# Kernel tuning notes

Hardware: AMD Instinct MI355X
Metric: run time of the kernel (lower is better)

The kernel has to match this reference:

```python
import jax, jax.numpy as jnp
import numpy as np

N_STATES = 12
N_SUBJECTS = 100
N_CHANNELS = 64
BATCH = 32
SEQ = 1024
LAMBDA_MU = 1.0
LAMBDA_L = 1.0


def _make_chol(key, shape):
    # valid lower-triangular Cholesky factors with positive diagonal
    a = jax.random.normal(key, shape, dtype=jnp.float32) * 0.05
    eye = jnp.eye(shape[-1], dtype=jnp.float32)
    return jnp.tril(a) + eye


def setup_inputs() -> dict:
    key = jax.random.key(0)
    ks = jax.random.split(key, 7)
    data = jax.random.normal(ks[0], (BATCH, SEQ, N_CHANNELS), dtype=jnp.float32)
    mu_pop = jax.random.normal(ks[1], (N_STATES, N_CHANNELS), dtype=jnp.float32)
    L_pop = _make_chol(ks[2], (N_STATES, N_CHANNELS, N_CHANNELS))
    mu_subj = jax.random.normal(ks[3], (N_SUBJECTS, N_STATES, N_CHANNELS), dtype=jnp.float32)
    L_subj = _make_chol(ks[4], (N_SUBJECTS, N_STATES, N_CHANNELS, N_CHANNELS))
    gamma = jax.random.uniform(ks[5], (BATCH, SEQ, N_STATES), dtype=jnp.float32)
    gamma = gamma / jnp.sum(gamma, axis=-1, keepdims=True)  # responsibilities sum to 1
    subject_ids = jax.random.randint(ks[6], (BATCH, 1), 0, N_SUBJECTS, dtype=jnp.int32)
    return {"data": data, "mu_pop": mu_pop, "L_pop": L_pop,
            "mu_subj": mu_subj, "L_subj": L_subj, "gamma": gamma,
            "subject_ids": subject_ids}


def reference(data, mu_pop, L_pop, mu_subj, L_subj, gamma, subject_ids):
    sid = subject_ids.reshape(-1).astype(jnp.int32)            # (B,)
    mu_b = mu_subj[sid]                                        # (B,K,C)
    L_b = L_subj[sid]                                          # (B,K,C,C)

    C = data.shape[-1]
    # diff[b,k,c,t] = data[b,t,c] - mu_b[b,k,c]  -> (B,K,C,T)
    diff = jnp.transpose(data, (0, 2, 1))[:, None, :, :] - mu_b[:, :, :, None]
    # batched triangular solve: z = L^{-1} diff  (B,K,C,T)
    z = jax.lax.linalg.triangular_solve(L_b, diff, left_side=True, lower=True)
    quad = jnp.sum(z * z, axis=2)                              # (B,K,T)
    logdet = jnp.sum(jnp.log(jnp.diagonal(L_b, axis1=-2, axis2=-1)), axis=-1)  # (B,K)
    log_2pi = jnp.float32(np.log(2.0 * np.pi))
    log_probs = -0.5 * quad - logdet[:, :, None] - 0.5 * C * log_2pi  # (B,K,T)

    weighted_ll = jnp.einsum('btk,bkt->bt', gamma, log_probs)  # (B,T)
    # calculation == 'sum': sum over time, mean over batch
    ll = jnp.mean(jnp.sum(weighted_ll, axis=1))
    nll = -ll

    n_total = jnp.float32(mu_subj.shape[0])
    present = jnp.zeros((mu_subj.shape[0],), dtype=jnp.float32).at[sid].set(1.0)
    mu_reg = jnp.sum(present * jnp.sum((mu_subj - mu_pop[None]) ** 2, axis=(1, 2)))
    L_reg = jnp.sum(present * jnp.sum((L_subj - L_pop[None]) ** 2, axis=(1, 2, 3)))
    scale = jnp.sum(present) / n_total
    reg = (LAMBDA_MU / 2.0 * mu_reg + LAMBDA_L / 2.0 * L_reg) * scale

    total = nll + reg
    return total[None]  # shape (1,), matching tf.expand_dims(total_loss, -1)
```

## Files before the change

### kernel.cpp

```cpp
#include <hip/hip_runtime.h>
#include <math.h>

#define NB 32
#define NT 1024
#define NK 12
#define NC 64
#define NS 100
#define SOLVE_BLOCKS (NB * NK * 4)
#define REG_BLOCKS (NS * NK)


__global__ __launch_bounds__(128) void init_kernel(int* __restrict__ present) {
  int tid = threadIdx.x;
  if (tid < NS) present[tid] = 0;
}

template <int C>
struct Row {
  static __device__ __forceinline__ void run(float (&z)[NC],
                                             const float4* __restrict__ Ls4,
                                             float& quad) {
    float a0 = z[C];
    float a1 = 0.0f;
    float diag = 0.0f;
#pragma unroll
    for (int g = 0; g <= C / 4; ++g) {
      float4 v = Ls4[C * 16 + g];
#pragma unroll
      for (int e = 0; e < 4; ++e) {
        int j = 4 * g + e;
        float ve = (e == 0) ? v.x : (e == 1) ? v.y : (e == 2) ? v.z : v.w;
        if (j < C) {
          if (j & 1)
            a1 = fmaf(-ve, z[j], a1);
          else
            a0 = fmaf(-ve, z[j], a0);
        } else if (j == C) {
          diag = ve;
        }
      }
    }
    float zc = (a0 + a1) * __builtin_amdgcn_rcpf(diag);
    z[C] = zc;
    quad = fmaf(zc, zc, quad);
    Row<C + 1>::run(z, Ls4, quad);
  }
};
template <>
struct Row<NC> {
  static __device__ __forceinline__ void run(float (&)[NC], const float4*,
                                             float&) {}
};

__global__ __launch_bounds__(256) void solve_kernel(
    const float* __restrict__ data,
    const float* __restrict__ mu_subj,
    const float* __restrict__ L_subj,
    const float* __restrict__ gamma,
    const int*   __restrict__ sids,
    float*       __restrict__ solve_part,
    int*         __restrict__ present) {
  int blk  = blockIdx.x;
  int x    = blk & 7;
  int r    = blk >> 3;
  int b    = (r / 48) * 8 + x;
  int kt   = r % 48;
  int k    = kt >> 2;
  int tile = kt & 3;
  int tid  = threadIdx.x;
  int lane = tid & 63;
  int t    = tile * 256 + tid;

  int sid = __builtin_amdgcn_readfirstlane(sids[b]);
  if (tid == 0 && k == 0 && tile == 0) present[sid] = 1;

  const float* __restrict__ Lb = L_subj + (size_t)(sid * NK + k) * (NC * NC);
  const float* __restrict__ mu = mu_subj + (size_t)(sid * NK + k) * NC;

  __shared__ float4 Ls4[NC * NC / 4];
  const float4* Lg = reinterpret_cast<const float4*>(Lb);
#pragma unroll
  for (int i = 0; i < 4; ++i) Ls4[tid + 256 * i] = Lg[tid + 256 * i];
  __syncthreads();

  const float* Lsf = reinterpret_cast<const float*>(Ls4);
  float ld = __logf(Lsf[lane * (NC + 1)]);
#pragma unroll
  for (int off = 1; off < 64; off <<= 1) ld += __shfl_xor(ld, off);

  float z[NC];
  const float4* dp =
      reinterpret_cast<const float4*>(data + ((size_t)b * NT + t) * NC);
#pragma unroll
  for (int i = 0; i < NC / 4; ++i) {
    float4 v = dp[i];
    z[4 * i + 0] = v.x - mu[4 * i + 0];
    z[4 * i + 1] = v.y - mu[4 * i + 1];
    z[4 * i + 2] = v.z - mu[4 * i + 2];
    z[4 * i + 3] = v.w - mu[4 * i + 3];
  }

  float quad = 0.0f;
  Row<0>::run(z, Ls4, quad);

  float g = gamma[((size_t)b * NT + t) * NK + k];
  float w = g * (-0.5f * quad - ld);

#pragma unroll
  for (int off = 1; off < 64; off <<= 1) w += __shfl_xor(w, off);

  __shared__ float red[4];
  if (lane == 0) red[tid >> 6] = w;
  __syncthreads();
  if (tid == 0) solve_part[blockIdx.x] = red[0] + red[1] + red[2] + red[3];
}

__global__ __launch_bounds__(256) void reg_kernel(
    const float* __restrict__ mu_pop,
    const float* __restrict__ L_pop,
    const float* __restrict__ mu_subj,
    const float* __restrict__ L_subj,
    const int*   __restrict__ present,
    float*       __restrict__ mu_part,
    float*       __restrict__ L_part) {
  int bid = blockIdx.x;
  int s = bid / NK;
  int k = bid % NK;
  int tid = threadIdx.x;
  if (present[s] == 0) {
    if (tid == 0) {
      mu_part[bid] = 0.0f;
      L_part[bid] = 0.0f;
    }
    return;
  }

  const float4* Ls =
      reinterpret_cast<const float4*>(L_subj + (size_t)(s * NK + k) * (NC * NC));
  const float4* Lp =
      reinterpret_cast<const float4*>(L_pop + (size_t)k * (NC * NC));
  float sl = 0.0f;
#pragma unroll
  for (int i = 0; i < 4; ++i) {
    int idx = tid + i * 256;
    float4 a = Ls[idx], p = Lp[idx];
    float dx = a.x - p.x, dy = a.y - p.y, dz = a.z - p.z, dw = a.w - p.w;
    sl += dx * dx + dy * dy + dz * dz + dw * dw;
  }
  float sm = 0.0f;
  if (tid < NC) {
    float d = mu_subj[(size_t)(s * NK + k) * NC + tid] - mu_pop[k * NC + tid];
    sm = d * d;
  }
#pragma unroll
  for (int off = 1; off < 64; off <<= 1) {
    sl += __shfl_xor(sl, off);
    sm += __shfl_xor(sm, off);
  }
  __shared__ float rl[4], rm[4];
  int lane = tid & 63;
  if (lane == 0) {
    rl[tid >> 6] = sl;
    rm[tid >> 6] = sm;
  }
  __syncthreads();
  if (tid == 0) {
    mu_part[bid] = rm[0] + rm[1] + rm[2] + rm[3];
    L_part[bid] = rl[0] + rl[1] + rl[2] + rl[3];
  }
}

__global__ __launch_bounds__(256) void finalize_kernel(
    const float* __restrict__ solve_part, const float* __restrict__ mu_part,
    const float* __restrict__ L_part, const int* __restrict__ present,
    float* __restrict__ out) {
  int tid = threadIdx.x;
  double s_ll = 0.0, s_mu = 0.0, s_L = 0.0;
  for (int i = tid; i < SOLVE_BLOCKS; i += 256) s_ll += (double)solve_part[i];
  for (int i = tid; i < REG_BLOCKS; i += 256) {
    s_mu += (double)mu_part[i];
    s_L += (double)L_part[i];
  }
  int cnt = (tid < NS) ? present[tid] : 0;
#pragma unroll
  for (int off = 1; off < 64; off <<= 1) {
    s_ll += __shfl_xor(s_ll, off);
    s_mu += __shfl_xor(s_mu, off);
    s_L += __shfl_xor(s_L, off);
    cnt += __shfl_xor(cnt, off);
  }
  __shared__ double r0[4], r1[4], r2[4];
  __shared__ int r3[4];
  int lane = tid & 63;
  if (lane == 0) {
    r0[tid >> 6] = s_ll;
    r1[tid >> 6] = s_mu;
    r2[tid >> 6] = s_L;
    r3[tid >> 6] = cnt;
  }
  __syncthreads();
  if (tid == 0) {
    double ll_sum = r0[0] + r0[1] + r0[2] + r0[3];
    double mu_reg = r1[0] + r1[1] + r1[2] + r1[3];
    double L_reg = r2[0] + r2[1] + r2[2] + r2[3];
    int c = r3[0] + r3[1] + r3[2] + r3[3];
    double c0 = 0.5 * (double)NC * log(2.0 * M_PI);
    double ll = ll_sum / (double)NB - (double)NT * c0;
    double reg = (0.5 * mu_reg + 0.5 * L_reg) * ((double)c / (double)NS);
    out[0] = (float)(-ll + reg);
  }
}

extern "C" void kernel_launch(void* const* d_in, const int* in_sizes, int n_in,
                              void* d_out, int out_size, void* d_ws,
                              size_t ws_size, hipStream_t stream) {
  const float* data    = (const float*)d_in[0];
  const float* mu_pop  = (const float*)d_in[1];
  const float* L_pop   = (const float*)d_in[2];
  const float* mu_subj = (const float*)d_in[3];
  const float* L_subj  = (const float*)d_in[4];
  const float* gamma   = (const float*)d_in[5];
  const int*   sids    = (const int*)d_in[6];
  float* out = (float*)d_out;

  float* solve_part = (float*)d_ws;
  float* mu_part    = solve_part + SOLVE_BLOCKS;
  float* L_part     = mu_part + REG_BLOCKS;
  int*   present    = (int*)(L_part + REG_BLOCKS);

  hipLaunchKernelGGL(init_kernel, dim3(1), dim3(128), 0, stream, present);
  hipLaunchKernelGGL(solve_kernel, dim3(SOLVE_BLOCKS), dim3(256), 0, stream,
                     data, mu_subj, L_subj, gamma, sids, solve_part, present);
  hipLaunchKernelGGL(reg_kernel, dim3(REG_BLOCKS), dim3(256), 0, stream,
                     mu_pop, L_pop, mu_subj, L_subj, present, mu_part, L_part);
  hipLaunchKernelGGL(finalize_kernel, dim3(1), dim3(256), 0, stream,
                     solve_part, mu_part, L_part, present, out);
}
```

Baseline: 49.46 us.

## Replace per-timestep triangular solve with explicit inverse and bf16 MFMA matmul

A new kernel inverts each selected Cholesky factor (one per batch and state) by forward substitution on identity columns and stores the inverse in bf16 in workspace. The main kernel then computes z = L^{-1}(x-mu) with 16x16x32 bf16 MFMA instructions instead of a serial 64-row scalar solve per thread. It also computes the squared norm from the accumulators. This trades the O(C^2) dependent FMA chain for matrix-core throughput, at the cost of an extra launch, workspace traffic and bf16 rounding of both the inverse and the centred data, which lowers accuracy.

After: 44.91 us. -9.2%, faster.

```diff
diff --git a/kernel.cpp b/kernel.cpp
--- a/kernel.cpp
+++ b/kernel.cpp
@@ -9,6 +9,15 @@
 #define SOLVE_BLOCKS (NB * NK * 4)
 #define REG_BLOCKS (NS * NK)
 
+typedef __attribute__((ext_vector_type(8))) short short8v;
+typedef __attribute__((ext_vector_type(4))) float f32x4;
+
+
+__device__ __forceinline__ short f2bf(float f) {
+  union { float f; unsigned u; } v{f};
+  unsigned r = v.u + 0x7fffu + ((v.u >> 16) & 1u);
+  return (short)(r >> 16);
+}
 
 __global__ __launch_bounds__(128) void init_kernel(int* __restrict__ present) {
   int tid = threadIdx.x;
@@ -52,77 +61,154 @@
                                              float&) {}
 };
 
-__global__ __launch_bounds__(256) void solve_kernel(
+__global__ __launch_bounds__(64) void invert_kernel(
+    const float* __restrict__ L_subj, const int* __restrict__ sids,
+    unsigned short* __restrict__ Wws) {
+  int b = blockIdx.x / NK;
+  int k = blockIdx.x % NK;
+  int j = threadIdx.x;
+  int sid = __builtin_amdgcn_readfirstlane(sids[b]);
+
+  __shared__ float4 Ls4[NC * NC / 4];
+  const float4* Lg =
+      reinterpret_cast<const float4*>(L_subj + (size_t)(sid * NK + k) * NC * NC);
+#pragma unroll
+  for (int i = 0; i < 16; ++i) Ls4[j + 64 * i] = Lg[j + 64 * i];
+  __syncthreads();
+
+  float z[NC];
+#pragma unroll
+  for (int c = 0; c < NC; ++c) z[c] = (c == j) ? 1.0f : 0.0f;
+  float dummy = 0.0f;
+  Row<0>::run(z, Ls4, dummy);
+
+  __shared__ float Wlds[NC * (NC + 1)];
+#pragma unroll
+  for (int r = 0; r < NC; ++r) Wlds[r * (NC + 1) + j] = z[r];
+  __syncthreads();
+
+  const float* wr = Wlds + j * (NC + 1);
+  unsigned* dst =
+      reinterpret_cast<unsigned*>(Wws + (size_t)(b * NK + k) * NC * NC) + j * 32;
+#pragma unroll
+  for (int i = 0; i < 32; ++i) {
+    unsigned lo = (unsigned short)f2bf(wr[2 * i]);
+    unsigned hi = (unsigned short)f2bf(wr[2 * i + 1]);
+    dst[i] = lo | (hi << 16);
+  }
+}
+
+__global__ __launch_bounds__(64) void mfma_kernel(
     const float* __restrict__ data,
     const float* __restrict__ mu_subj,
     const float* __restrict__ L_subj,
     const float* __restrict__ gamma,
     const int*   __restrict__ sids,
-    float*       __restrict__ solve_part,
-    int*         __restrict__ present) {
-  int blk  = blockIdx.x;
-  int x    = blk & 7;
-  int r    = blk >> 3;
-  int b    = (r / 48) * 8 + x;
-  int kt   = r % 48;
-  int k    = kt >> 2;
-  int tile = kt & 3;
-  int tid  = threadIdx.x;
-  int lane = tid & 63;
-  int t    = tile * 256 + tid;
+    const unsigned short* __restrict__ Wws,
+    float* __restrict__ solve_part,
+    int*   __restrict__ present) {
+  int blk = blockIdx.x;
+  int x   = blk & 7;
+  int r   = blk >> 3;
+  int b   = (r / 48) * 8 + x;
+  int rem = r % 48;
+  int k   = rem >> 2;
+  int q   = rem & 3;
+  int lane = threadIdx.x;
+  int g = lane >> 4;
+  int m = lane & 15;
 
   int sid = __builtin_amdgcn_readfirstlane(sids[b]);
-  if (tid == 0 && k == 0 && tile == 0) present[sid] = 1;
-
-  const float* __restrict__ Lb = L_subj + (size_t)(sid * NK + k) * (NC * NC);
-  const float* __restrict__ mu = mu_subj + (size_t)(sid * NK + k) * NC;
-
-  __shared__ float4 Ls4[NC * NC / 4];
-  const float4* Lg = reinterpret_cast<const float4*>(Lb);
-#pragma unroll
-  for (int i = 0; i < 4; ++i) Ls4[tid + 256 * i] = Lg[tid + 256 * i];
-  __syncthreads();
-
-  const float* Lsf = reinterpret_cast<const float*>(Ls4);
-  float ld = __logf(Lsf[lane * (NC + 1)]);
+  if (lane == 0 && k == 0 && q == 0) present[sid] = 1;
+
+  const float* Lb = L_subj + (size_t)(sid * NK + k) * NC * NC;
+  float ld = __logf(Lb[lane * (NC + 1)]);
 #pragma unroll
   for (int off = 1; off < 64; off <<= 1) ld += __shfl_xor(ld, off);
 
-  float z[NC];
-  const float4* dp =
-      reinterpret_cast<const float4*>(data + ((size_t)b * NT + t) * NC);
-#pragma unroll
-  for (int i = 0; i < NC / 4; ++i) {
-    float4 v = dp[i];
-    z[4 * i + 0] = v.x - mu[4 * i + 0];
-    z[4 * i + 1] = v.y - mu[4 * i + 1];
-    z[4 * i + 2] = v.z - mu[4 * i + 2];
-    z[4 * i + 3] = v.w - mu[4 * i + 3];
-  }
-
-  float quad = 0.0f;
-  Row<0>::run(z, Ls4, quad);
-
-  float g = gamma[((size_t)b * NT + t) * NK + k];
-  float w = g * (-0.5f * quad - ld);
-
-#pragma unroll
-  for (int off = 1; off < 64; off <<= 1) w += __shfl_xor(w, off);
-
-  __shared__ float red[4];
-  if (lane == 0) red[tid >> 6] = w;
-  __syncthreads();
-  if (tid == 0) solve_part[blockIdx.x] = red[0] + red[1] + red[2] + red[3];
+  const unsigned short* Wp = Wws + (size_t)(b * NK + k) * NC * NC;
+  short8v afrag[4][2];
+#pragma unroll
+  for (int ct = 0; ct < 4; ++ct)
+#pragma unroll
+    for (int kk = 0; kk < 2; ++kk)
+      afrag[ct][kk] = *reinterpret_cast<const short8v*>(
+          Wp + (ct * 16 + m) * NC + kk * 32 + g * 8);
+
+  const float* mu = mu_subj + (size_t)(sid * NK + k) * NC;
+  float4 mu0a = *reinterpret_cast<const float4*>(mu + g * 8);
+  float4 mu0b = *reinterpret_cast<const float4*>(mu + g * 8 + 4);
+  float4 mu1a = *reinterpret_cast<const float4*>(mu + 32 + g * 8);
+  float4 mu1b = *reinterpret_cast<const float4*>(mu + 32 + g * 8 + 4);
+
+  float wacc = 0.0f;
+  int t0 = q * 256;
+#pragma unroll 2
+  for (int tt = 0; tt < 16; ++tt) {
+    int t = t0 + tt * 16 + m;
+    const float* dp = data + ((size_t)(b * NT + t)) * NC;
+
+    short8v bf0, bf1;
+    {
+      const float4* dv = reinterpret_cast<const float4*>(dp + g * 8);
+      float4 v0 = dv[0], v1 = dv[1];
+      bf0[0] = f2bf(v0.x - mu0a.x);
+      bf0[1] = f2bf(v0.y - mu0a.y);
+      bf0[2] = f2bf(v0.z - mu0a.z);
+      bf0[3] = f2bf(v0.w - mu0a.w);
+      bf0[4] = f2bf(v1.x - mu0b.x);
+      bf0[5] = f2bf(v1.y - mu0b.y);
+      bf0[6] = f2bf(v1.z - mu0b.z);
+      bf0[7] = f2bf(v1.w - mu0b.w);
+    }
+    {
+      const float4* dv = reinterpret_cast<const float4*>(dp + 32 + g * 8);
+      float4 v0 = dv[0], v1 = dv[1];
+      bf1[0] = f2bf(v0.x - mu1a.x);
+      bf1[1] = f2bf(v0.y - mu1a.y);
+      bf1[2] = f2bf(v0.z - mu1a.z);
+      bf1[3] = f2bf(v0.w - mu1a.w);
+      bf1[4] = f2bf(v1.x - mu1b.x);
+      bf1[5] = f2bf(v1.y - mu1b.y);
+      bf1[6] = f2bf(v1.z - mu1b.z);
+      bf1[7] = f2bf(v1.w - mu1b.w);
+    }
+
+    f32x4 acc0 = {0.f, 0.f, 0.f, 0.f}, acc1 = acc0, acc2 = acc0, acc3 = acc0;
+    acc0 = __builtin_amdgcn_mfma_f32_16x16x32_bf16(afrag[0][0], bf0, acc0, 0, 0, 0);
+    acc0 = __builtin_amdgcn_mfma_f32_16x16x32_bf16(afrag[0][1], bf1, acc0, 0, 0, 0);
+    acc1 = __builtin_amdgcn_mfma_f32_16x16x32_bf16(afrag[1][0], bf0, acc1, 0, 0, 0);
+    acc1 = __builtin_amdgcn_mfma_f32_16x16x32_bf16(afrag[1][1], bf1, acc1, 0, 0, 0);
+    acc2 = __builtin_amdgcn_mfma_f32_16x16x32_bf16(afrag[2][0], bf0, acc2, 0, 0, 0);
+    acc2 = __builtin_amdgcn_mfma_f32_16x16x32_bf16(afrag[2][1], bf1, acc2, 0, 0, 0);
+    acc3 = __builtin_amdgcn_mfma_f32_16x16x32_bf16(afrag[3][0], bf0, acc3, 0, 0, 0);
+    acc3 = __builtin_amdgcn_mfma_f32_16x16x32_bf16(afrag[3][1], bf1, acc3, 0, 0, 0);
+
+    float s = 0.0f;
+#pragma unroll
+    for (int e = 0; e < 4; ++e) {
+      s = fmaf(acc0[e], acc0[e], s);
+      s = fmaf(acc1[e], acc1[e], s);
+      s = fmaf(acc2[e], acc2[e], s);
+      s = fmaf(acc3[e], acc3[e], s);
+    }
+    s += __shfl_xor(s, 16);
+    s += __shfl_xor(s, 32);
+
+    float gam = gamma[((size_t)(b * NT + t)) * NK + k];
+    wacc = fmaf(gam, -0.5f * s - ld, wacc);
+  }
+
+#pragma unroll
+  for (int off = 1; off < 64; off <<= 1) wacc += __shfl_xor(wacc, off);
+  if (lane == 0) solve_part[blockIdx.x] = wacc * 0.25f;
 }
 
 __global__ __launch_bounds__(256) void reg_kernel(
-    const float* __restrict__ mu_pop,
-    const float* __restrict__ L_pop,
-    const float* __restrict__ mu_subj,
-    const float* __restrict__ L_subj,
-    const int*   __restrict__ present,
-    float*       __restrict__ mu_part,
-    float*       __restrict__ L_part) {
+    const float* __restrict__ mu_pop, const float* __restrict__ L_pop,
+    const float* __restrict__ mu_subj, const float* __restrict__ L_subj,
+    const int* __restrict__ present, float* __restrict__ mu_part,
+    float* __restrict__ L_part) {
   int bid = blockIdx.x;
   int s = bid / NK;
   int k = bid % NK;
@@ -136,9 +222,9 @@
   }
 
   const float4* Ls =
-      reinterpret_cast<const float4*>(L_subj + (size_t)(s * NK + k) * (NC * NC));
+      reinterpret_cast<const float4*>(L_subj + (size_t)(s * NK + k) * NC * NC);
   const float4* Lp =
-      reinterpret_cast<const float4*>(L_pop + (size_t)k * (NC * NC));
+      reinterpret_cast<const float4*>(L_pop + (size_t)k * NC * NC);
   float sl = 0.0f;
 #pragma unroll
   for (int i = 0; i < 4; ++i) {
@@ -223,14 +309,18 @@
   const int*   sids    = (const int*)d_in[6];
   float* out = (float*)d_out;
 
-  float* solve_part = (float*)d_ws;
+  unsigned short* Wws = (unsigned short*)d_ws;
+  float* solve_part = (float*)((char*)d_ws + (size_t)NB * NK * NC * NC * 2);
   float* mu_part    = solve_part + SOLVE_BLOCKS;
   float* L_part     = mu_part + REG_BLOCKS;
   int*   present    = (int*)(L_part + REG_BLOCKS);
 
   hipLaunchKernelGGL(init_kernel, dim3(1), dim3(128), 0, stream, present);
-  hipLaunchKernelGGL(solve_kernel, dim3(SOLVE_BLOCKS), dim3(256), 0, stream,
-                     data, mu_subj, L_subj, gamma, sids, solve_part, present);
+  hipLaunchKernelGGL(invert_kernel, dim3(NB * NK), dim3(64), 0, stream,
+                     L_subj, sids, Wws);
+  hipLaunchKernelGGL(mfma_kernel, dim3(SOLVE_BLOCKS), dim3(64), 0, stream,
+                     data, mu_subj, L_subj, gamma, sids, Wws, solve_part,
+                     present);
   hipLaunchKernelGGL(reg_kernel, dim3(REG_BLOCKS), dim3(256), 0, stream,
                      mu_pop, L_pop, mu_subj, L_subj, present, mu_part, L_part);
   hipLaunchKernelGGL(finalize_kernel, dim3(1), dim3(256), 0, stream,
```
